# Optimization experiments

Hardware: AMD Instinct MI355X
Metric: run time of the kernel (lower is better)

Reference implementation:

```python
import jax, jax.numpy as jnp
import numpy as np
from jax import lax

H = 16          # attention heads
N_LAYERS = 2    # encoder applies the SAME (shared-weight) layer N times
FILTERS = (1, 3, 5)
EPS_LN = 1e-6
EPS_BN = 1e-5


def _ln(x, a, b):
    # torch LayerNorm variant: unbiased std, eps added to std (not var)
    m = x.mean(-1, keepdims=True)
    s = jnp.std(x, axis=-1, keepdims=True, ddof=1)
    return a * (x - m) / (s + EPS_LN) + b


def _mha(x, wq, bq, wk, bk, wv, bv, wo, bo):
    B, S, D = x.shape
    dk = D // H
    def proj(w, b):
        return (x @ w + b).reshape(B, S, H, dk).transpose(0, 2, 1, 3)  # bhsd
    q, k, v = proj(wq, bq), proj(wk, bk), proj(wv, bv)
    scores = jnp.einsum('bhqd,bhkd->bhqk', q, k) / jnp.sqrt(jnp.float32(dk))
    p = jax.nn.softmax(scores, axis=-1)  # dropout is identity in eval mode
    o = jnp.einsum('bhqk,bhkd->bhqd', p, v)
    o = o.transpose(0, 2, 1, 3).reshape(B, S, D)
    return o @ wo + bo


def _conv_branch(xt, w, b, g, beta, m, v):
    # xt: [B, C, L]; w: [out, in, f]; BatchNorm1d in eval mode (running stats)
    f = w.shape[-1]
    y = lax.conv_general_dilated(xt, w, window_strides=(1,),
                                 padding=[(f // 2, f // 2)],
                                 dimension_numbers=('NCH', 'OIH', 'NCH'))
    y = y + b[None, :, None]
    y = (y - m[None, :, None]) / jnp.sqrt(v[None, :, None] + EPS_BN)
    y = y * g[None, :, None] + beta[None, :, None]
    return jax.nn.relu(y)


def setup_inputs() -> dict:
    key = jax.random.key(0)
    B, S, D = 8, 1024, 1024
    ks = iter(jax.random.split(key, 64))
    nrm = lambda shape, sc=0.02: jax.random.normal(next(ks), shape, jnp.float32) * sc
    inp = {'x': jax.random.normal(next(ks), (B, S, D), jnp.float32)}
    for nm in ('wq', 'wk', 'wv', 'wo'):
        inp[nm] = nrm((D, D))
    for nm in ('bq', 'bk', 'bv', 'bo'):
        inp[nm] = nrm((D,), 0.01)
    for i, f in enumerate(FILTERS, 1):
        inp[f'conv_w{i}'] = nrm((D, D, f))
        inp[f'conv_b{i}'] = nrm((D,), 0.01)
        inp[f'bn_g{i}'] = 1.0 + nrm((D,), 0.05)
        inp[f'bn_b{i}'] = nrm((D,), 0.05)
        inp[f'bn_m{i}'] = nrm((D,), 0.1)
        inp[f'bn_v{i}'] = 1.0 + 0.1 * jax.random.uniform(next(ks), (D,), jnp.float32)
    for nm in ('ln1_a', 'ln2_a', 'lnf_a'):
        inp[nm] = jnp.ones((D,), jnp.float32)
    for nm in ('ln1_b', 'ln2_b', 'lnf_b'):
        inp[nm] = jnp.zeros((D,), jnp.float32)
    return inp


def reference(x, wq, bq, wk, bk, wv, bv, wo, bo,
              conv_w1, conv_b1, bn_g1, bn_b1, bn_m1, bn_v1,
              conv_w2, conv_b2, bn_g2, bn_b2, bn_m2, bn_v2,
              conv_w3, conv_b3, bn_g3, bn_b3, bn_m3, bn_v3,
              ln1_a, ln1_b, ln2_a, ln2_b, lnf_a, lnf_b):
    convs = ((conv_w1, conv_b1, bn_g1, bn_b1, bn_m1, bn_v1),
             (conv_w2, conv_b2, bn_g2, bn_b2, bn_m2, bn_v2),
             (conv_w3, conv_b3, bn_g3, bn_b3, bn_m3, bn_v3))

    def ffn(h):
        xt = h.transpose(0, 2, 1)  # [B, D, S]
        outs = [_conv_branch(xt, *p) for p in convs]
        out = sum(outs) / jnp.float32(len(outs))  # mean over branch ensemble
        return out.transpose(0, 2, 1)

    for _ in range(N_LAYERS):  # shared-weight layer applied N times
        x = x + _mha(_ln(x, ln1_a, ln1_b), wq, bq, wk, bk, wv, bv, wo, bo)
        x = x + ffn(_ln(x, ln2_a, ln2_b))
    return _ln(x, lnf_a, lnf_b)
```

## Files before the change

### kernel.cpp

```cpp
#include <hip/hip_runtime.h>

#define TPB 256

typedef __attribute__((ext_vector_type(4))) float f32x4;
typedef __attribute__((ext_vector_type(8))) short s16x8;

__device__ __forceinline__ ushort f2bf(float f) {
  unsigned x = __float_as_uint(f);
  return (ushort)((x + 0x7fffu + ((x >> 16) & 1u)) >> 16);
}
__device__ __forceinline__ float b2f(ushort u) {
  return __uint_as_float(((unsigned)u) << 16);
}
__device__ __forceinline__ void gload_lds16(const ushort* g, ushort* l) {
  __builtin_amdgcn_global_load_lds(
      (const __attribute__((address_space(1))) void*)g,
      (__attribute__((address_space(3))) void*)l, 16, 0, 0);
}

__device__ __forceinline__ float blk_sum(float v, float* red, int tid) {
#pragma unroll
  for (int o = 32; o; o >>= 1) v += __shfl_xor(v, o);
  if ((tid & 63) == 0) red[tid >> 6] = v;
  __syncthreads();
  float r = red[0] + red[1] + red[2] + red[3];
  __syncthreads();
  return r;
}

template<bool C_BF16, bool HAS_BIAS, bool HAS_RES>
__global__ __launch_bounds__(TPB, 2)
void gemm_bt(const ushort* __restrict__ A, int lda,
             const ushort* __restrict__ B, int ldb,
             void* __restrict__ Cp, int ldc,
             const float* __restrict__ bias, const float* __restrict__ Res, int K)
{
  constexpr int BM = 128, BK = 32;
  __shared__ ushort lA[BM * BK];
  __shared__ ushort lB[128 * BK];
  const int tid = threadIdx.x;
  const int rowBase = blockIdx.x * BM;
  const int colBase = blockIdx.y * 128;
  const int w = tid >> 6, lane = tid & 63;
  const int wr = w >> 1, wc = w & 1;
  const int lr = lane & 15, lk = (lane >> 4) * 8;

  f32x4 acc[4][4] = {};

  for (int k0 = 0; k0 < K; k0 += BK) {
#pragma unroll
    for (int i = 0; i < 2; ++i) {
      int idx = i * TPB + tid;
      int r = idx >> 2, kk = (idx & 3) * 8;
      gload_lds16(A + (long)(rowBase + r) * lda + k0 + kk, &lA[idx * 8]);
    }
#pragma unroll
    for (int i = 0; i < 2; ++i) {
      int idx = i * TPB + tid;
      int r = idx >> 2, kk = (idx & 3) * 8;
      gload_lds16(B + (long)(colBase + r) * ldb + k0 + kk, &lB[idx * 8]);
    }
    __syncthreads();
    s16x8 af[4], bfr[4];
#pragma unroll
    for (int m = 0; m < 4; ++m)
      af[m] = *(const s16x8*)&lA[(wr * 64 + m * 16 + lr) * BK + lk];
#pragma unroll
    for (int n = 0; n < 4; ++n)
      bfr[n] = *(const s16x8*)&lB[(wc * 64 + n * 16 + lr) * BK + lk];
#pragma unroll
    for (int m = 0; m < 4; ++m)
#pragma unroll
      for (int n = 0; n < 4; ++n)
        acc[m][n] = __builtin_amdgcn_mfma_f32_16x16x32_bf16(af[m], bfr[n], acc[m][n], 0, 0, 0);
    __syncthreads();
  }

  const int crow0 = rowBase + wr * 64 + (lane >> 4) * 4;
#pragma unroll
  for (int m = 0; m < 4; ++m) {
#pragma unroll
    for (int n = 0; n < 4; ++n) {
      const int ccol = colBase + wc * 64 + n * 16 + lr;
      const float bv = HAS_BIAS ? bias[ccol] : 0.f;
#pragma unroll
      for (int j = 0; j < 4; ++j) {
        const long off = (long)(crow0 + m * 16 + j) * ldc + ccol;
        float v = acc[m][n][j] + bv;
        if (HAS_RES) v += Res[off];
        if (C_BF16) ((ushort*)Cp)[off] = f2bf(v);
        else        ((float*)Cp)[off] = v;
      }
    }
  }
}

__global__ __launch_bounds__(512, 2)
void conv_fused2(const ushort* __restrict__ A, const ushort* __restrict__ W9,
                 float* __restrict__ x, const float* __restrict__ sc,
                 const float* __restrict__ sh, const ushort* __restrict__ zp)
{
  extern __shared__ ushort smem[];
  ushort* lA = smem;
  ushort* lB = smem + 49152;
  const int tid = threadIdx.x;
  const int rowBase = blockIdx.x * 256;
  const int colBase = blockIdx.y * 128;
  const int w = tid >> 6, lane = tid & 63;
  const int wrm = w >> 1, wcn = w & 1;
  const int lr = lane & 15, kg = lane >> 4;

  f32x4 acc[4][4] = {};
  f32x4 res[4][4] = {};

  auto stage = [&](int t, int buf) {
    const int s = t >> 4;
    const int k0 = (t & 15) * 64;
    const int shift = (s == 0) ? 0 : ((s <= 3) ? s - 2 : s - 6);
    const ushort* Wseg = W9 + (long)s * 1048576 + k0;
    const ushort* Ak = A + k0;
    ushort* dA = lA + buf * 16384;
    ushort* dB = lB + buf * 8192;
#pragma unroll
    for (int i = 0; i < 4; ++i) {
      int li = i * 512 + tid;
      int r = li >> 3, sl = li & 7;
      int gsl = sl ^ (r & 7);
      int gr = rowBase + r;
      int sr = (gr & 1023) + shift;
      const ushort* src = ((unsigned)sr < 1024u)
          ? (Ak + (long)((gr & ~1023) + sr) * 1024 + gsl * 8) : zp;
      gload_lds16(src, dA + li * 8);
    }
#pragma unroll
    for (int i = 0; i < 2; ++i) {
      int li = i * 512 + tid;
      int r = li >> 3, sl = li & 7;
      int gsl = sl ^ (r & 7);
      gload_lds16(Wseg + (long)(colBase + r) * 1024 + gsl * 8, dB + li * 8);
    }
  };

  stage(0, 0);
  stage(1, 1);
  __builtin_amdgcn_sched_barrier(0);
  asm volatile("s_waitcnt vmcnt(6)" ::: "memory");
  __builtin_amdgcn_sched_barrier(0);
  __syncthreads();

#pragma unroll 3
  for (int t = 0; t < 144; ++t) {
    const int cur = t % 3;
    if (t + 2 < 144) stage(t + 2, (t + 2) % 3);

    const ushort* bA = lA + cur * 16384;
    const ushort* bB = lB + cur * 8192;
#pragma unroll
    for (int ks = 0; ks < 2; ++ks) {
      s16x8 af[4], bfr[4];
#pragma unroll
      for (int mf = 0; mf < 4; ++mf) {
        int r = wrm * 64 + mf * 16 + lr;
        int sl = (ks * 4 + kg) ^ (r & 7);
        af[mf] = *(const s16x8*)&bA[r * 64 + sl * 8];
      }
#pragma unroll
      for (int nf = 0; nf < 4; ++nf) {
        int r = wcn * 64 + nf * 16 + lr;
        int sl = (ks * 4 + kg) ^ (r & 7);
        bfr[nf] = *(const s16x8*)&bB[r * 64 + sl * 8];
      }
      __builtin_amdgcn_s_setprio(1);
#pragma unroll
      for (int mf = 0; mf < 4; ++mf)
#pragma unroll
        for (int nf = 0; nf < 4; ++nf)
          acc[mf][nf] = __builtin_amdgcn_mfma_f32_16x16x32_bf16(af[mf], bfr[nf], acc[mf][nf], 0, 0, 0);
      __builtin_amdgcn_s_setprio(0);
    }

    if (t == 15 || t == 63 || t == 143) {
      const int br = (t == 15) ? 0 : (t == 63 ? 1 : 2);
#pragma unroll
      for (int nf = 0; nf < 4; ++nf) {
        const int col = colBase + wcn * 64 + nf * 16 + lr;
        const float scv = sc[br * 1024 + col];
        const float shv = sh[br * 1024 + col];
#pragma unroll
        for (int mf = 0; mf < 4; ++mf)
#pragma unroll
          for (int j = 0; j < 4; ++j) {
            res[mf][nf][j] += fmaxf(acc[mf][nf][j] * scv + shv, 0.f);
            acc[mf][nf][j] = 0.f;
          }
      }
    }

    __builtin_amdgcn_sched_barrier(0);
    if (t + 2 < 144)      asm volatile("s_waitcnt vmcnt(6)" ::: "memory");
    else if (t + 1 < 144) asm volatile("s_waitcnt vmcnt(0)" ::: "memory");
    __builtin_amdgcn_sched_barrier(0);
    __syncthreads();
  }

  const int crow0 = rowBase + wrm * 64 + kg * 4;
#pragma unroll
  for (int mf = 0; mf < 4; ++mf)
#pragma unroll
    for (int nf = 0; nf < 4; ++nf) {
      const int col = colBase + wcn * 64 + nf * 16 + lr;
#pragma unroll
      for (int j = 0; j < 4; ++j) {
        const long off = (long)(crow0 + mf * 16 + j) * 1024 + col;
        x[off] += res[mf][nf][j] * (1.f / 3.f);
      }
    }
}

__global__ __launch_bounds__(TPB)
void flash_attn(const ushort* __restrict__ qkv, const ushort* __restrict__ vt,
                ushort* __restrict__ obuf)
{
  __shared__ ushort lK[2][64 * 64];
  __shared__ ushort lVt[2][64 * 64];
  __shared__ ushort lP[4 * 32 * 64];
  const int tid = threadIdx.x;
  const int w = tid >> 6, lane = tid & 63;
  const int g = lane >> 4, c = lane & 15;
  const int bh = blockIdx.y, b = bh >> 4, h = bh & 15;
  const int qw = blockIdx.x * 128 + w * 32;
  const float c8 = 0.18033688f;

  auto stage = [&](int t, int pb) {
    const int kv0 = t * 64;
#pragma unroll
    for (int i = 0; i < 2; ++i) {
      int idx = i * TPB + tid;
      int r = idx >> 3, dc = (idx & 7) * 8;
      gload_lds16(qkv + (long)((b << 10) + kv0 + r) * 3072 + 1024 + (h << 6) + dc,
                  &lK[pb][idx * 8]);
    }
#pragma unroll
    for (int i = 0; i < 2; ++i) {
      int idx = i * TPB + tid;
      int r = idx >> 3, dc = (idx & 7) * 8;
      gload_lds16(vt + (long)((bh << 6) + r) * 1024 + kv0 + dc, &lVt[pb][idx * 8]);
    }
  };

  s16x8 qfr[2][2];
#pragma unroll
  for (int qf = 0; qf < 2; ++qf)
#pragma unroll
    for (int ds = 0; ds < 2; ++ds)
      qfr[qf][ds] = *(const s16x8*)(qkv
          + (long)((b << 10) + qw + qf * 16 + c) * 3072 + (h << 6) + ds * 32 + g * 8);

  f32x4 acc_o[2][4] = {};
  float m[2][4], l[2][4];
#pragma unroll
  for (int qf = 0; qf < 2; ++qf)
#pragma unroll
    for (int j = 0; j < 4; ++j) { m[qf][j] = -3.0e38f; l[qf][j] = 0.f; }

  ushort* lPw = &lP[w * 2048];

  stage(0, 0);
  __builtin_amdgcn_sched_barrier(0);
  asm volatile("s_waitcnt vmcnt(0)" ::: "memory");
  __builtin_amdgcn_sched_barrier(0);
  __syncthreads();

  for (int t = 0; t < 16; ++t) {
    const int pb = t & 1;
    if (t + 1 < 16) stage(t + 1, pb ^ 1);

    f32x4 s[2][4] = {};
#pragma unroll
    for (int ds = 0; ds < 2; ++ds) {
      s16x8 bk[4];
#pragma unroll
      for (int kf = 0; kf < 4; ++kf)
        bk[kf] = *(const s16x8*)&lK[pb][(kf * 16 + c) * 64 + ds * 32 + g * 8];
      __builtin_amdgcn_s_setprio(1);
#pragma unroll
      for (int qf = 0; qf < 2; ++qf)
#pragma unroll
        for (int kf = 0; kf < 4; ++kf)
          s[qf][kf] = __builtin_amdgcn_mfma_f32_16x16x32_bf16(qfr[qf][ds], bk[kf], s[qf][kf], 0, 0, 0);
      __builtin_amdgcn_s_setprio(0);
    }

#pragma unroll
    for (int qf = 0; qf < 2; ++qf)
#pragma unroll
      for (int j = 0; j < 4; ++j) {
        float tm = fmaxf(fmaxf(s[qf][0][j], s[qf][1][j]), fmaxf(s[qf][2][j], s[qf][3][j]));
        tm = fmaxf(tm, __shfl_xor(tm, 1));
        tm = fmaxf(tm, __shfl_xor(tm, 2));
        tm = fmaxf(tm, __shfl_xor(tm, 4));
        tm = fmaxf(tm, __shfl_xor(tm, 8));
        float mn = fmaxf(m[qf][j], tm);
        float scale = exp2f((m[qf][j] - mn) * c8);
        m[qf][j] = mn;
        l[qf][j] *= scale;
#pragma unroll
        for (int df = 0; df < 4; ++df) acc_o[qf][df][j] *= scale;
        float ps = 0.f;
#pragma unroll
        for (int kf = 0; kf < 4; ++kf) {
          float pv = exp2f((s[qf][kf][j] - mn) * c8);
          ps += pv;
          lPw[(qf * 16 + g * 4 + j) * 64 + kf * 16 + c] = f2bf(pv);
        }
        l[qf][j] += ps;
      }

#pragma unroll
    for (int kvb = 0; kvb < 2; ++kvb) {
      s16x8 pA[2], vB[4];
#pragma unroll
      for (int qf = 0; qf < 2; ++qf)
        pA[qf] = *(const s16x8*)&lPw[(qf * 16 + c) * 64 + kvb * 32 + g * 8];
#pragma unroll
      for (int df = 0; df < 4; ++df)
        vB[df] = *(const s16x8*)&lVt[pb][(df * 16 + c) * 64 + kvb * 32 + g * 8];
      __builtin_amdgcn_s_setprio(1);
#pragma unroll
      for (int qf = 0; qf < 2; ++qf)
#pragma unroll
        for (int df = 0; df < 4; ++df)
          acc_o[qf][df] = __builtin_amdgcn_mfma_f32_16x16x32_bf16(pA[qf], vB[df], acc_o[qf][df], 0, 0, 0);
      __builtin_amdgcn_s_setprio(0);
    }

    __builtin_amdgcn_sched_barrier(0);
    asm volatile("s_waitcnt vmcnt(0)" ::: "memory");
    __builtin_amdgcn_sched_barrier(0);
    __syncthreads();
  }

#pragma unroll
  for (int qf = 0; qf < 2; ++qf)
#pragma unroll
    for (int j = 0; j < 4; ++j) {
      float lv = l[qf][j];
      lv += __shfl_xor(lv, 1);
      lv += __shfl_xor(lv, 2);
      lv += __shfl_xor(lv, 4);
      lv += __shfl_xor(lv, 8);
      float inv = 1.f / lv;
#pragma unroll
      for (int df = 0; df < 4; ++df)
        obuf[(long)((b << 10) + qw + qf * 16 + g * 4 + j) * 1024 + (h << 6) + df * 16 + c]
            = f2bf(acc_o[qf][df][j] * inv);
    }
}

template<bool OBF>
__global__ __launch_bounds__(TPB)
void ln_rows(const float* __restrict__ X, const float* __restrict__ ga,
             const float* __restrict__ gb, void* __restrict__ out)
{
  __shared__ float red[4];
  const int tid = threadIdx.x;
  const long base = (long)blockIdx.x * 1024;
  f32x4 v = *(const f32x4*)&X[base + tid * 4];
  float mean = blk_sum(v[0] + v[1] + v[2] + v[3], red, tid) * (1.f / 1024.f);
  f32x4 d = v - mean;
  float qs = blk_sum(d[0]*d[0] + d[1]*d[1] + d[2]*d[2] + d[3]*d[3], red, tid);
  float inv = 1.f / (sqrtf(qs * (1.f / 1023.f)) + 1e-6f);
  f32x4 a4 = *(const f32x4*)&ga[tid * 4];
  f32x4 b4 = *(const f32x4*)&gb[tid * 4];
  f32x4 r = a4 * (d * inv) + b4;
  if (OBF) {
    ushort4 o4 = { f2bf(r[0]), f2bf(r[1]), f2bf(r[2]), f2bf(r[3]) };
    *(ushort4*)((ushort*)out + base + tid * 4) = o4;
  } else {
    *(f32x4*)((float*)out + base + tid * 4) = r;
  }
}

__global__ __launch_bounds__(TPB)
void vt_build(const ushort* __restrict__ qkv, ushort* __restrict__ vt)
{
  __shared__ ushort t[64][72];
  const int tid = threadIdx.x;
  const int bh = blockIdx.y, b = bh >> 4, h = bh & 15;
  const int kv0 = blockIdx.x * 64;
#pragma unroll
  for (int it = 0; it < 2; ++it) {
    int idx = (it * TPB + tid) * 8;
    int r = idx >> 6, cc = idx & 63;
    s16x8 v = *(const s16x8*)(qkv + ((long)((b << 10) + kv0 + r)) * 3072 + 2048 + (h << 6) + cc);
#pragma unroll
    for (int j = 0; j < 8; ++j) t[r][cc + j] = (ushort)v[j];
  }
  __syncthreads();
#pragma unroll
  for (int it = 0; it < 2; ++it) {
    int idx = (it * TPB + tid) * 8;
    int dd = idx >> 6, kvo = idx & 63;
    ushort tmp[8];
#pragma unroll
    for (int j = 0; j < 8; ++j) tmp[j] = t[kvo + j][dd];
    *(s16x8*)(vt + ((long)bh * 64 + dd) * 1024 + kv0 + kvo) = *(const s16x8*)tmp;
  }
}

__global__ __launch_bounds__(TPB)
void wt_build(const float* __restrict__ in, ushort* __restrict__ out)
{
  __shared__ float t[64][65];
  const int tid = threadIdx.x;
  const int k0 = blockIdx.x * 64, n0 = blockIdx.y * 64;
#pragma unroll
  for (int it = 0; it < 4; ++it) {
    int idx = it * TPB + tid;
    int r = idx >> 4, c4 = (idx & 15) * 4;
    f32x4 v = *(const f32x4*)&in[(long)(k0 + r) * 1024 + n0 + c4];
    t[r][c4] = v[0]; t[r][c4 + 1] = v[1]; t[r][c4 + 2] = v[2]; t[r][c4 + 3] = v[3];
  }
  __syncthreads();
#pragma unroll
  for (int it = 0; it < 4; ++it) {
    int idx = it * TPB + tid;
    int nr = idx >> 4, k4 = (idx & 15) * 4;
    ushort4 o = { f2bf(t[k4][nr]), f2bf(t[k4 + 1][nr]),
                  f2bf(t[k4 + 2][nr]), f2bf(t[k4 + 3][nr]) };
    *(ushort4*)&out[(long)(n0 + nr) * 1024 + k0 + k4] = o;
  }
}
__global__ __launch_bounds__(TPB)
void tap_build(const float* __restrict__ w, ushort* __restrict__ out, int f)
{
  long oi = (long)blockIdx.x * TPB + threadIdx.x;
  for (int t = 0; t < f; ++t)
    out[(long)t * 1048576 + oi] = f2bf(w[oi * f + t]);
}
__global__ __launch_bounds__(TPB)
void bn_prep(const float* __restrict__ cb, const float* __restrict__ g,
             const float* __restrict__ bb, const float* __restrict__ m,
             const float* __restrict__ v, float* __restrict__ sc, float* __restrict__ sh)
{
  int i = blockIdx.x * TPB + threadIdx.x;
  float s = g[i] * rsqrtf(v[i] + 1e-5f);
  sc[i] = s;
  sh[i] = (cb[i] - m[i]) * s + bb[i];
}
__global__ __launch_bounds__(TPB)
void qkvb_build(const float* __restrict__ bq, const float* __restrict__ bk,
                const float* __restrict__ bv, float* __restrict__ out)
{
  int i = blockIdx.x * TPB + threadIdx.x;
  out[i] = (i < 1024) ? bq[i] : (i < 2048 ? bk[i - 1024] : bv[i - 2048]);
}
__global__ void zero_ws(ushort* z) { z[threadIdx.x] = 0; }

extern "C" void kernel_launch(void* const* d_in, const int* in_sizes, int n_in,
                              void* d_out, int out_size, void* d_ws, size_t ws_size,
                              hipStream_t stream)
{
  const float* X  = (const float*)d_in[0];
  const float* Wq = (const float*)d_in[1];
  const float* Wk = (const float*)d_in[2];
  const float* Wv = (const float*)d_in[3];
  const float* Wo = (const float*)d_in[4];
  const float* Bq = (const float*)d_in[5];
  const float* Bk = (const float*)d_in[6];
  const float* Bv = (const float*)d_in[7];
  const float* Bo = (const float*)d_in[8];
  const float *CW[3], *CB[3], *BG[3], *BBe[3], *BMu[3], *BVa[3];
  for (int i = 0; i < 3; ++i) {
    CW[i]  = (const float*)d_in[9 + 6 * i];
    CB[i]  = (const float*)d_in[10 + 6 * i];
    BG[i]  = (const float*)d_in[11 + 6 * i];
    BBe[i] = (const float*)d_in[12 + 6 * i];
    BMu[i] = (const float*)d_in[13 + 6 * i];
    BVa[i] = (const float*)d_in[14 + 6 * i];
  }
  const float* L1a = (const float*)d_in[27];
  const float* L2a = (const float*)d_in[28];
  const float* LFa = (const float*)d_in[29];
  const float* L1b = (const float*)d_in[30];
  const float* L2b = (const float*)d_in[31];
  const float* LFb = (const float*)d_in[32];

  char* p = (char*)d_ws;
  auto carve = [&](size_t bytes) { char* r = p; p += (bytes + 255) & ~(size_t)255; return r; };
  ushort* abuf  = (ushort*)carve(16777216);
  ushort* wqkvt = (ushort*)carve(6291456);
  ushort* wot   = (ushort*)carve(2097152);
  ushort* wtap  = (ushort*)carve(18874368);
  ushort* qkv   = (ushort*)carve(50331648);
  ushort* vt    = (ushort*)carve(16777216);
  ushort* obuf  = (ushort*)carve(16777216);
  float*  qkvb  = (float*) carve(12288);
  float*  bnsc  = (float*) carve(12288);
  float*  bnsh  = (float*) carve(12288);
  ushort* zp    = (ushort*)carve(256);
  if ((size_t)(p - (char*)d_ws) > ws_size) return;

  float* xbuf = (float*)d_out;

  wt_build<<<dim3(16, 16), TPB, 0, stream>>>(Wq, wqkvt);
  wt_build<<<dim3(16, 16), TPB, 0, stream>>>(Wk, wqkvt + 1048576);
  wt_build<<<dim3(16, 16), TPB, 0, stream>>>(Wv, wqkvt + 2097152);
  wt_build<<<dim3(16, 16), TPB, 0, stream>>>(Wo, wot);
  tap_build<<<4096, TPB, 0, stream>>>(CW[0], wtap, 1);
  tap_build<<<4096, TPB, 0, stream>>>(CW[1], wtap + 1048576, 3);
  tap_build<<<4096, TPB, 0, stream>>>(CW[2], wtap + 4 * 1048576, 5);
  for (int i = 0; i < 3; ++i)
    bn_prep<<<4, TPB, 0, stream>>>(CB[i], BG[i], BBe[i], BMu[i], BVa[i],
                                   bnsc + i * 1024, bnsh + i * 1024);
  qkvb_build<<<12, TPB, 0, stream>>>(Bq, Bk, Bv, qkvb);
  zero_ws<<<1, 128, 0, stream>>>(zp);

  for (int L = 0; L < 2; ++L) {
    const float* xs = (L == 0) ? X : xbuf;
    ln_rows<true><<<8192, TPB, 0, stream>>>(xs, L1a, L1b, abuf);
    gemm_bt<true, true, false><<<dim3(64, 24), TPB, 0, stream>>>(
        abuf, 1024, wqkvt, 1024, qkv, 3072, qkvb, nullptr, 1024);
    vt_build<<<dim3(16, 128), TPB, 0, stream>>>(qkv, vt);
    flash_attn<<<dim3(8, 128), TPB, 0, stream>>>(qkv, vt, obuf);
    gemm_bt<false, true, true><<<dim3(64, 8), TPB, 0, stream>>>(
        obuf, 1024, wot, 1024, xbuf, 1024, Bo, xs, 1024);
    ln_rows<true><<<8192, TPB, 0, stream>>>(xbuf, L2a, L2b, abuf);
    conv_fused2<<<dim3(32, 8), 512, 147456, stream>>>(abuf, wtap, xbuf, bnsc, bnsh, zp);
  }
  ln_rows<false><<<8192, TPB, 0, stream>>>(xbuf, LFa, LFb, d_out);
}
```

Baseline: 990.6 us.

## Replace QKV/output GEMM with triple-buffered 256x128 tile kernel using swizzled LDS

Replaces the simple single-buffered 128x128 GEMM with a 512-thread 256x128 tile kernel. It stages BK=64 slices into a three-deep LDS ring with async global-to-LDS loads and XOR-swizzles the LDS layout to avoid bank conflicts. It also raises wave priority around the MFMA bursts. The goal is to overlap memory loads with matrix math and cut LDS conflicts and barrier stalls in the projection GEMMs. The cost is a large dynamic shared-memory footprint (147 KB) and fewer blocks in the grid, which lowers occupancy and wave count.

New measurement: 1.001 ms. No clear change (+1.1%).

```diff
diff --git a/kernel.cpp b/kernel.cpp
--- a/kernel.cpp
+++ b/kernel.cpp
@@ -29,70 +29,107 @@
 }
 
 template<bool C_BF16, bool HAS_BIAS, bool HAS_RES>
-__global__ __launch_bounds__(TPB, 2)
-void gemm_bt(const ushort* __restrict__ A, int lda,
-             const ushort* __restrict__ B, int ldb,
-             void* __restrict__ Cp, int ldc,
-             const float* __restrict__ bias, const float* __restrict__ Res, int K)
-{
-  constexpr int BM = 128, BK = 32;
-  __shared__ ushort lA[BM * BK];
-  __shared__ ushort lB[128 * BK];
+__global__ __launch_bounds__(512, 2)
+void gemm_bt2(const ushort* __restrict__ A, int lda,
+              const ushort* __restrict__ B, int ldb,
+              void* __restrict__ Cp, int ldc,
+              const float* __restrict__ bias, const float* __restrict__ Res,
+              int K)
+{
+  extern __shared__ ushort smem[];
+  ushort* lA = smem;
+  ushort* lB = smem + 49152;
   const int tid = threadIdx.x;
-  const int rowBase = blockIdx.x * BM;
+  const int rowBase = blockIdx.x * 256;
   const int colBase = blockIdx.y * 128;
   const int w = tid >> 6, lane = tid & 63;
-  const int wr = w >> 1, wc = w & 1;
-  const int lr = lane & 15, lk = (lane >> 4) * 8;
+  const int wrm = w >> 1, wcn = w & 1;
+  const int lr = lane & 15, kg = lane >> 4;
+  const int nsteps = K >> 6;
 
   f32x4 acc[4][4] = {};
 
-  for (int k0 = 0; k0 < K; k0 += BK) {
+  auto stage = [&](int t, int buf) {
+    const int k0 = t * 64;
+    ushort* dA = lA + buf * 16384;
+    ushort* dB = lB + buf * 8192;
+#pragma unroll
+    for (int i = 0; i < 4; ++i) {
+      int li = i * 512 + tid;
+      int r = li >> 3, sl = li & 7;
+      int gsl = sl ^ (r & 7);
+      gload_lds16(A + (long)(rowBase + r) * lda + k0 + gsl * 8, dA + li * 8);
+    }
 #pragma unroll
     for (int i = 0; i < 2; ++i) {
-      int idx = i * TPB + tid;
-      int r = idx >> 2, kk = (idx & 3) * 8;
-      gload_lds16(A + (long)(rowBase + r) * lda + k0 + kk, &lA[idx * 8]);
-    }
-#pragma unroll
-    for (int i = 0; i < 2; ++i) {
-      int idx = i * TPB + tid;
-      int r = idx >> 2, kk = (idx & 3) * 8;
-      gload_lds16(B + (long)(colBase + r) * ldb + k0 + kk, &lB[idx * 8]);
-    }
+      int li = i * 512 + tid;
+      int r = li >> 3, sl = li & 7;
+      int gsl = sl ^ (r & 7);
+      gload_lds16(B + (long)(colBase + r) * ldb + k0 + gsl * 8, dB + li * 8);
+    }
+  };
+
+  stage(0, 0);
+  stage(1, 1);
+  __builtin_amdgcn_sched_barrier(0);
+  asm volatile("s_waitcnt vmcnt(6)" ::: "memory");
+  __builtin_amdgcn_sched_barrier(0);
+  __syncthreads();
+
+#pragma unroll 3
+  for (int t = 0; t < nsteps; ++t) {
+    const int cur = t % 3;
+    if (t + 2 < nsteps) stage(t + 2, (t + 2) % 3);
+
+    const ushort* bA = lA + cur * 16384;
+    const ushort* bB = lB + cur * 8192;
+#pragma unroll
+    for (int ks = 0; ks < 2; ++ks) {
+      s16x8 af[4], bfr[4];
+#pragma unroll
+      for (int mf = 0; mf < 4; ++mf) {
+        int r = wrm * 64 + mf * 16 + lr;
+        int sl = (ks * 4 + kg) ^ (r & 7);
+        af[mf] = *(const s16x8*)&bA[r * 64 + sl * 8];
+      }
+#pragma unroll
+      for (int nf = 0; nf < 4; ++nf) {
+        int r = wcn * 64 + nf * 16 + lr;
+        int sl = (ks * 4 + kg) ^ (r & 7);
+        bfr[nf] = *(const s16x8*)&bB[r * 64 + sl * 8];
+      }
+      __builtin_amdgcn_s_setprio(1);
+#pragma unroll
+      for (int mf = 0; mf < 4; ++mf)
+#pragma unroll
+        for (int nf = 0; nf < 4; ++nf)
+          acc[mf][nf] = __builtin_amdgcn_mfma_f32_16x16x32_bf16(af[mf], bfr[nf], acc[mf][nf], 0, 0, 0);
+      __builtin_amdgcn_s_setprio(0);
+    }
+
+    __builtin_amdgcn_sched_barrier(0);
+    if (t + 2 < nsteps)      asm volatile("s_waitcnt vmcnt(6)" ::: "memory");
+    else if (t + 1 < nsteps) asm volatile("s_waitcnt vmcnt(0)" ::: "memory");
+    __builtin_amdgcn_sched_barrier(0);
     __syncthreads();
-    s16x8 af[4], bfr[4];
-#pragma unroll
-    for (int m = 0; m < 4; ++m)
-      af[m] = *(const s16x8*)&lA[(wr * 64 + m * 16 + lr) * BK + lk];
-#pragma unroll
-    for (int n = 0; n < 4; ++n)
-      bfr[n] = *(const s16x8*)&lB[(wc * 64 + n * 16 + lr) * BK + lk];
-#pragma unroll
-    for (int m = 0; m < 4; ++m)
-#pragma unroll
-      for (int n = 0; n < 4; ++n)
-        acc[m][n] = __builtin_amdgcn_mfma_f32_16x16x32_bf16(af[m], bfr[n], acc[m][n], 0, 0, 0);
-    __syncthreads();
-  }
-
-  const int crow0 = rowBase + wr * 64 + (lane >> 4) * 4;
-#pragma unroll
-  for (int m = 0; m < 4; ++m) {
-#pragma unroll
-    for (int n = 0; n < 4; ++n) {
-      const int ccol = colBase + wc * 64 + n * 16 + lr;
-      const float bv = HAS_BIAS ? bias[ccol] : 0.f;
+  }
+
+  const int crow0 = rowBase + wrm * 64 + kg * 4;
+#pragma unroll
+  for (int mf = 0; mf < 4; ++mf)
+#pragma unroll
+    for (int nf = 0; nf < 4; ++nf) {
+      const int col = colBase + wcn * 64 + nf * 16 + lr;
+      const float bv = HAS_BIAS ? bias[col] : 0.f;
 #pragma unroll
       for (int j = 0; j < 4; ++j) {
-        const long off = (long)(crow0 + m * 16 + j) * ldc + ccol;
-        float v = acc[m][n][j] + bv;
+        const long off = (long)(crow0 + mf * 16 + j) * ldc + col;
+        float v = acc[mf][nf][j] + bv;
         if (HAS_RES) v += Res[off];
         if (C_BF16) ((ushort*)Cp)[off] = f2bf(v);
         else        ((float*)Cp)[off] = v;
       }
     }
-  }
 }
 
 __global__ __launch_bounds__(512, 2)
@@ -519,11 +556,11 @@
   for (int L = 0; L < 2; ++L) {
     const float* xs = (L == 0) ? X : xbuf;
     ln_rows<true><<<8192, TPB, 0, stream>>>(xs, L1a, L1b, abuf);
-    gemm_bt<true, true, false><<<dim3(64, 24), TPB, 0, stream>>>(
+    gemm_bt2<true, true, false><<<dim3(32, 24), 512, 147456, stream>>>(
         abuf, 1024, wqkvt, 1024, qkv, 3072, qkvb, nullptr, 1024);
     vt_build<<<dim3(16, 128), TPB, 0, stream>>>(qkv, vt);
     flash_attn<<<dim3(8, 128), TPB, 0, stream>>>(qkv, vt, obuf);
-    gemm_bt<false, true, true><<<dim3(64, 8), TPB, 0, stream>>>(
+    gemm_bt2<false, true, true><<<dim3(32, 8), 512, 147456, stream>>>(
         obuf, 1024, wot, 1024, xbuf, 1024, Bo, xs, 1024);
     ln_rows<true><<<8192, TPB, 0, stream>>>(xbuf, L2a, L2b, abuf);
     conv_fused2<<<dim3(32, 8), 512, 147456, stream>>>(abuf, wtap, xbuf, bnsc, bnsh, zp);
```
